# Kernel optimization log

Hardware: AMD Instinct MI355X
Metric: run time of the kernel (lower is better)

Reference implementation:

```python
import jax, jax.numpy as jnp
import numpy as np

B, N, D, H, K, L, BLOCKS = 8, 256, 768, 12, 128, 4, 2
HD = D // H
SCALING = HD ** -0.5
NEG = -1e9  # stand-in for -inf; exp underflows to exactly 0 in softmax


def layernorm(x, s, b):
    m = x.mean(-1, keepdims=True)
    v = ((x - m) ** 2).mean(-1, keepdims=True)
    return (x - m) * jax.lax.rsqrt(v + 1e-5) * s + b


def _gauss(x, mean, std):
    a = (2.0 * 3.14159) ** 0.5
    return jnp.exp(-0.5 * ((x - mean) / std) ** 2) / (a * std)


def setup_inputs() -> dict:
    key = jax.random.key(0)
    ks = jax.random.split(key, 16)
    nrm = lambda k, shape: jax.random.normal(k, shape, jnp.float32) * 0.02
    atoms = jax.random.randint(ks[0], (B, N), 0, 10, dtype=jnp.int32)
    pos = jax.random.normal(ks[1], (B, N, 3), jnp.float32)
    atom_emb = nrm(ks[2], (10, D)).at[0].set(0.0)  # padding_idx=0
    gbf_means = jax.random.uniform(ks[3], (K,), jnp.float32, 0.0, 3.0)
    gbf_stds = jax.random.uniform(ks[4], (K,), jnp.float32, 0.0, 3.0)
    gbf_mul = jnp.ones((100, 1), jnp.float32)
    gbf_bias = jnp.zeros((100, 1), jnp.float32)
    bp_w1 = nrm(ks[5], (K, K)); bp_b1 = jnp.zeros((K,), jnp.float32)
    bp_w2 = nrm(ks[6], (K, H)); bp_b2 = jnp.zeros((H,), jnp.float32)
    edge_w = nrm(ks[7], (K, D)); edge_b = jnp.zeros((D,), jnp.float32)
    ap_w = nrm(ks[8], (D, D)); ap_b = jnp.zeros((D,), jnp.float32)
    ln1_s = jnp.ones((L, D), jnp.float32); ln1_b = jnp.zeros((L, D), jnp.float32)
    wi = nrm(ks[9], (L, D, 3 * D)); bi = jnp.zeros((L, 3 * D), jnp.float32)
    wo = nrm(ks[10], (L, D, D)); bo = jnp.zeros((L, D), jnp.float32)
    ln2_s = jnp.ones((L, D), jnp.float32); ln2_b = jnp.zeros((L, D), jnp.float32)
    w1 = nrm(ks[11], (L, D, D)); b1 = jnp.zeros((L, D), jnp.float32)
    w2 = nrm(ks[12], (L, D, D)); b2 = jnp.zeros((L, D), jnp.float32)
    fln_s = jnp.ones((D,), jnp.float32); fln_b = jnp.zeros((D,), jnp.float32)
    return dict(atoms=atoms, pos=pos, atom_emb=atom_emb, gbf_means=gbf_means,
                gbf_stds=gbf_stds, gbf_mul=gbf_mul, gbf_bias=gbf_bias,
                bp_w1=bp_w1, bp_b1=bp_b1, bp_w2=bp_w2, bp_b2=bp_b2,
                edge_w=edge_w, edge_b=edge_b, ap_w=ap_w, ap_b=ap_b,
                ln1_s=ln1_s, ln1_b=ln1_b, wi=wi, bi=bi, wo=wo, bo=bo,
                ln2_s=ln2_s, ln2_b=ln2_b, w1=w1, b1=b1, w2=w2, b2=b2,
                fln_s=fln_s, fln_b=fln_b)


def reference(atoms, pos, atom_emb, gbf_means, gbf_stds, gbf_mul, gbf_bias,
              bp_w1, bp_b1, bp_w2, bp_b2, edge_w, edge_b, ap_w, ap_b,
              ln1_s, ln1_b, wi, bi, wo, bo, ln2_s, ln2_b, w1, b1, w2, b2,
              fln_s, fln_b):
    pad = atoms == 0  # [B,N]
    delta = pos[:, None, :, :] - pos[:, :, None, :]  # [B,N,N,3]
    sq = (delta * delta).sum(-1)
    dist = jnp.where(sq > 0, jnp.sqrt(jnp.where(sq > 0, sq, 1.0)), 0.0)  # safe sqrt
    et = atoms[:, :, None] * 10 + atoms[:, None, :]  # [B,N,N] in [0,100)
    e = gbf_mul[et] * dist[..., None] + gbf_bias[et]  # [B,N,N,1]
    gbf = _gauss(e, gbf_means, jnp.abs(gbf_stds) + 1e-5)  # [B,N,N,K]
    # zero out padded j-columns, sum over j -> per-node edge feature
    ef = jnp.where(pad[:, None, :, None], 0.0, gbf).sum(axis=2)  # [B,N,K]
    node = atom_emb[atoms] + ef @ edge_w + edge_b  # [B,N,D]
    x = jnp.swapaxes(node, 0, 1) @ ap_w + ap_b  # [N,B,D]
    # attention bias: K-dim Gaussian features -> per-head bias
    bias = jax.nn.gelu(gbf @ bp_w1 + bp_b1, approximate=False) @ bp_w2 + bp_b2  # [B,N,N,H]
    bias = jnp.transpose(bias, (0, 3, 1, 2))  # [B,H,N,N]
    bias = jnp.where(pad[:, None, None, :], NEG, bias)

    def body(x, p):
        s1, c1, Wi, Bi, Wo, Bo, s2, c2, W1, B1, W2, B2 = p
        h = layernorm(x, s1, c1)
        q, k, v = jnp.split(h @ Wi + Bi, 3, axis=-1)
        q = q.reshape(N, B, H, HD) * SCALING
        k = k.reshape(N, B, H, HD)
        v = v.reshape(N, B, H, HD)
        sc = jnp.einsum('ibhd,jbhd->bhij', q, k) + bias
        pA = jax.nn.softmax(sc, axis=-1)
        o = jnp.einsum('bhij,jbhd->ibhd', pA, v).reshape(N, B, D)
        x = x + o @ Wo + Bo
        h = layernorm(x, s2, c2)
        h = jax.nn.gelu(h @ W1 + B1, approximate=False) @ W2 + B2
        return x + h, None

    stacked = (ln1_s, ln1_b, wi, bi, wo, bo, ln2_s, ln2_b, w1, b1, w2, b2)
    for _ in range(BLOCKS):
        x, _ = jax.lax.scan(body, x, stacked)
    x = layernorm(x, fln_s, fln_b)
    return jnp.swapaxes(x, 0, 1)  # [B,N,D]
```

## Files before the change

kernel.cpp:

```cpp
#include <hip/hip_runtime.h>
#include <math.h>

constexpr int Bn = 8, Nn = 256, Dn = 768, Hn = 12, Kn = 128;
constexpr int Tn = Nn * Bn;
constexpr float SCALE = 0.125f;
constexpr float NEGB = -1e9f;
constexpr float INV768 = 1.0f / 768.0f;

typedef __attribute__((ext_vector_type(8))) short bf16x8;
typedef __attribute__((ext_vector_type(4))) float f32x4;

#define MFMA16(a, b, c) __builtin_amdgcn_mfma_f32_16x16x32_bf16((a), (b), (c), 0, 0, 0)

__device__ __forceinline__ void gload_lds16(const void* g, void* l) {
  __builtin_amdgcn_global_load_lds(
      (const __attribute__((address_space(1))) void*)g,
      (__attribute__((address_space(3))) void*)l, 16, 0, 0);
}

__device__ __forceinline__ ushort f2bf(float x) {
  union { float f; unsigned u; } v; v.f = x;
  unsigned r = (v.u + 0x7fff + ((v.u >> 16) & 1)) >> 16;
  return (ushort)r;
}
__device__ __forceinline__ ushort f2bf_t(float x) {
  union { float f; unsigned u; } v; v.f = x;
  return (ushort)(v.u >> 16);
}
__device__ __forceinline__ float bf2f(ushort u) {
  union { unsigned u; float f; } v; v.u = ((unsigned)u) << 16;
  return v.f;
}
__device__ __forceinline__ float gelu_fast(float x) {
  float u = x * (0.7978845608f + 0.0356774081f * x * x);
  float e = __expf(2.0f * u);
  float t = 1.0f - 2.0f / (e + 1.0f);
  return 0.5f * x * (1.0f + t);
}
__device__ __forceinline__ float wave_sum(float v) {
#pragma unroll
  for (int off = 32; off; off >>= 1) v += __shfl_xor(v, off);
  return v;
}

__global__ __launch_bounds__(256) void wtrans(const float* __restrict__ W,
                                              ushort* __restrict__ WT,
                                              int Kd, int Nd) {
  __shared__ float tile[64][65];
  const float* Wl = W + (size_t)blockIdx.z * Kd * Nd;
  ushort* WTl = WT + (size_t)blockIdx.z * Kd * Nd;
  int n0 = blockIdx.x * 64, k0 = blockIdx.y * 64;
  int tid = threadIdx.x;
  for (int e = tid; e < 64 * 64; e += 256) {
    int r = e >> 6, c = e & 63;
    tile[r][c] = Wl[(size_t)(k0 + r) * Nd + n0 + c];
  }
  __syncthreads();
  for (int e = tid; e < 64 * 64; e += 256) {
    int r = e >> 6, c = e & 63;
    WTl[(size_t)(n0 + r) * Kd + k0 + c] = f2bf(tile[c][r]);
  }
}

__global__ __launch_bounds__(128) void ef_kernel(
    const int* __restrict__ atoms, const float* __restrict__ pos,
    const float* __restrict__ means, const float* __restrict__ stds,
    const float* __restrict__ gmul, const float* __restrict__ gbias,
    ushort* __restrict__ ef) {
  int i = blockIdx.x, b = blockIdx.y;
  __shared__ float sj[Nn];
  __shared__ int padm[Nn];
  int tid = threadIdx.x;
  int ai = atoms[b * Nn + i];
  float px = pos[(b * Nn + i) * 3], py = pos[(b * Nn + i) * 3 + 1], pz = pos[(b * Nn + i) * 3 + 2];
  for (int j = tid; j < Nn; j += 128) {
    int aj = atoms[b * Nn + j];
    float dx = px - pos[(b * Nn + j) * 3];
    float dy = py - pos[(b * Nn + j) * 3 + 1];
    float dz = pz - pos[(b * Nn + j) * 3 + 2];
    float sq = dx * dx + dy * dy + dz * dz;
    float d = sq > 0.f ? sqrtf(sq) : 0.f;
    int et = ai * 10 + aj;
    sj[j] = fmaf(gmul[et], d, gbias[et]);
    padm[j] = (aj == 0);
  }
  __syncthreads();
  int k = tid;
  float mean = means[k];
  float sd = fabsf(stds[k]) + 1e-5f;
  float inv = 1.0f / sd;
  float cn = inv * 0.3989423f;
  float acc = 0.f;
  for (int j = 0; j < Nn; ++j) {
    if (padm[j]) continue;
    float t = (sj[j] - mean) * inv;
    acc += __expf(-0.5f * t * t);
  }
  ef[(size_t)(b * Nn + i) * Kn + k] = f2bf(acc * cn);
}

__global__ __launch_bounds__(256) void gbias_kernel(
    const int* __restrict__ atoms, const float* __restrict__ pos,
    const float* __restrict__ means, const float* __restrict__ stds,
    const float* __restrict__ gmul, const float* __restrict__ gbias_,
    const ushort* __restrict__ w1T, const float* __restrict__ b1,
    const float* __restrict__ w2, const float* __restrict__ b2,
    ushort* __restrict__ biasb) {
  int i = blockIdx.x, b = blockIdx.y;
  __shared__ char W1s[32768];
  __shared__ char Ag[16384];
  __shared__ char W2s[4096];
  __shared__ float sj[256];
  __shared__ int pml[256];
  __shared__ float b1s[128], invs_[128], mui[128], cns[128];
  const int tid = threadIdx.x, w = tid >> 6, ln = tid & 63;
  const int frow = ln & 15, fgrp = ln >> 4;
  {
    int srow = ln >> 4, sc = ln & 15;
#pragma unroll
    for (int q = 0; q < 8; ++q) {
      int inst = w * 8 + q;
      int row = inst * 4 + srow;
      const char* g = (const char*)(w1T + row * 128) + ((sc * 16) ^ ((row & 7) << 4));
      gload_lds16(g, W1s + inst * 1024);
    }
  }
  if (tid < 128) {
    float mean = means[tid];
    float sd = fabsf(stds[tid]) + 1e-5f;
    float inv = 1.0f / sd;
    invs_[tid] = inv;
    mui[tid] = mean * inv;
    cns[tid] = inv * 0.3989423f;
    b1s[tid] = b1[tid];
  }
  for (int e = tid; e < 2048; e += 256) {
    int h = e >> 7, k = e & 127;
    float v = (h < 12) ? w2[k * 12 + h] : 0.f;
    *(ushort*)(W2s + h * 256 + ((2 * k) ^ ((h & 7) << 4))) = f2bf(v);
  }
  {
    int ai = atoms[b * Nn + i];
    int j = tid;
    int aj = atoms[b * Nn + j];
    float dx = pos[(b * Nn + i) * 3]     - pos[(b * Nn + j) * 3];
    float dy = pos[(b * Nn + i) * 3 + 1] - pos[(b * Nn + j) * 3 + 1];
    float dz = pos[(b * Nn + i) * 3 + 2] - pos[(b * Nn + j) * 3 + 2];
    float sq = dx * dx + dy * dy + dz * dz;
    float d = sq > 0.f ? sqrtf(sq) : 0.f;
    int et = ai * 10 + aj;
    sj[j] = fmaf(gmul[et], d, gbias_[et]);
    pml[j] = (aj == 0);
  }
  __syncthreads();

  for (int jt = 0; jt < 4; ++jt) {
    int j0 = jt * 64;
    {
      int k = tid & 127;
      float inv = invs_[k], mu = mui[k], cn = cns[k];
      int r0 = (tid >> 7) * 32;
#pragma unroll 8
      for (int rr = 0; rr < 32; ++rr) {
        int row = r0 + rr;
        float t = fmaf(inv, sj[j0 + row], -mu);
        float g = __expf(-0.5f * t * t) * cn;
        *(ushort*)(Ag + row * 256 + ((2 * k) ^ ((row & 7) << 4))) = f2bf_t(g);
      }
    }
    __syncthreads();
    f32x4 acc[8] = {};
    const int arow = w * 16 + frow;
#pragma unroll
    for (int ks = 0; ks < 4; ++ks) {
      bf16x8 af = *(const bf16x8*)(Ag + arow * 256 + ((ks * 64 + fgrp * 16) ^ ((arow & 7) << 4)));
#pragma unroll
      for (int nt = 0; nt < 8; ++nt) {
        int brow = nt * 16 + frow;
        bf16x8 bfv = *(const bf16x8*)(W1s + brow * 256 + ((ks * 64 + fgrp * 16) ^ ((brow & 7) << 4)));
        acc[nt] = MFMA16(af, bfv, acc[nt]);
      }
    }
    __syncthreads();
#pragma unroll
    for (int nt = 0; nt < 8; ++nt) {
      int n = nt * 16 + frow;
#pragma unroll
      for (int r = 0; r < 4; ++r) {
        int jloc = w * 16 + fgrp * 4 + r;
        float g = gelu_fast(acc[nt][r] + b1s[n]);
        *(ushort*)(Ag + jloc * 256 + ((2 * n) ^ ((jloc & 7) << 4))) = f2bf_t(g);
      }
    }
    __syncthreads();
    {
      f32x4 acc2 = {};
      int jrow = w * 16 + frow;
#pragma unroll
      for (int ks = 0; ks < 4; ++ks) {
        bf16x8 af = *(const bf16x8*)(Ag + jrow * 256 + ((ks * 64 + fgrp * 16) ^ ((jrow & 7) << 4)));
        bf16x8 bfv = *(const bf16x8*)(W2s + frow * 256 + ((ks * 64 + fgrp * 16) ^ ((frow & 7) << 4)));
        acc2 = MFMA16(af, bfv, acc2);
      }
      if (frow < 12) {
        float bv = b2[frow];
#pragma unroll
        for (int r = 0; r < 4; ++r) {
          int jl = w * 16 + fgrp * 4 + r;
          int jg = j0 + jl;
          float v = pml[jg] ? NEGB : (acc2[r] + bv);
          biasb[(((size_t)b * Hn + frow) * Nn + i) * Nn + jg] = f2bf(v);
        }
      }
    }
    __syncthreads();
  }
}

template <int MODE>
__global__ __launch_bounds__(256, 4) void mgemm(
    const ushort* __restrict__ A, const ushort* __restrict__ WT,
    const float* __restrict__ bias, const float* __restrict__ res,
    void* __restrict__ Cout, const int* __restrict__ atomsp,
    const float* __restrict__ embp, int M, int Kd, int Nd) {
  __shared__ char smem[16384];
  char* ldsA = smem;
  char* ldsB = smem + 8192;
  const int tid = threadIdx.x, w = tid >> 6, ln = tid & 63;
  const int m0 = blockIdx.y * 64, n0 = blockIdx.x * 64;
  const int wm = (w >> 1) * 32, wn = (w & 1) * 32;
  const int srow = ln >> 3, schunk = ln & 7;
  const int sswz = (schunk * 16) ^ (srow << 4);
  const int frow = ln & 15, fgrp = ln >> 4;
  f32x4 acc[2][2] = {};
  for (int kt = 0; kt < Kd; kt += 64) {
    __syncthreads();
#pragma unroll
    for (int q = 0; q < 2; ++q) {
      int r = (w * 2 + q) * 8 + srow;
      gload_lds16((const char*)(A + (size_t)(m0 + r) * Kd + kt) + sswz, ldsA + (w * 2 + q) * 1024);
    }
#pragma unroll
    for (int q = 0; q < 2; ++q) {
      int r = (w * 2 + q) * 8 + srow;
      gload_lds16((const char*)(WT + (size_t)(n0 + r) * Kd + kt) + sswz, ldsB + (w * 2 + q) * 1024);
    }
    __syncthreads();
#pragma unroll
    for (int ks = 0; ks < 2; ++ks) {
      bf16x8 af[2], bfv[2];
#pragma unroll
      for (int mt = 0; mt < 2; ++mt) {
        int row = wm + mt * 16 + frow;
        af[mt] = *(const bf16x8*)(ldsA + row * 128 + ((ks * 64 + fgrp * 16) ^ ((row & 7) << 4)));
      }
#pragma unroll
      for (int nt = 0; nt < 2; ++nt) {
        int row = wn + nt * 16 + frow;
        bfv[nt] = *(const bf16x8*)(ldsB + row * 128 + ((ks * 64 + fgrp * 16) ^ ((row & 7) << 4)));
      }
      acc[0][0] = MFMA16(af[0], bfv[0], acc[0][0]);
      acc[0][1] = MFMA16(af[0], bfv[1], acc[0][1]);
      acc[1][0] = MFMA16(af[1], bfv[0], acc[1][0]);
      acc[1][1] = MFMA16(af[1], bfv[1], acc[1][1]);
    }
  }
#pragma unroll
  for (int nt = 0; nt < 2; ++nt) {
    int n = n0 + wn + nt * 16 + frow;
    float bv = bias[n];
#pragma unroll
    for (int mt = 0; mt < 2; ++mt) {
#pragma unroll
      for (int r = 0; r < 4; ++r) {
        int m = m0 + wm + mt * 16 + fgrp * 4 + r;
        float v = acc[mt][nt][r] + bv;
        if (MODE == 1) v = gelu_fast(v);
        if (MODE == 2) v += res[(size_t)m * Nd + n];
        if (MODE == 5) v += embp[(size_t)atomsp[m] * Nd + n];
        if (MODE == 2 || MODE == 3) ((float*)Cout)[(size_t)m * Nd + n] = v;
        else                        ((ushort*)Cout)[(size_t)m * Nd + n] = f2bf(v);
      }
    }
  }
}

__global__ __launch_bounds__(256, 2) void mgemm128_qkv(
    const ushort* __restrict__ A, const ushort* __restrict__ WT,
    const float* __restrict__ bias, ushort* __restrict__ vTout,
    ushort* __restrict__ Cout, int M, int Kd, int Nd) {
  __shared__ char smem[32768];
  char* ldsA = smem;
  char* ldsB = smem + 16384;
  const int tid = threadIdx.x, w = tid >> 6, ln = tid & 63;
  const int m0 = blockIdx.y * 128, n0 = blockIdx.x * 128;
  const int wm = (w >> 1) * 64, wn = (w & 1) * 64;
  const int srow = ln >> 3, schunk = ln & 7;
  const int sswz = (schunk * 16) ^ (srow << 4);
  const int frow = ln & 15, fgrp = ln >> 4;
  f32x4 acc[4][4] = {};
  for (int kt = 0; kt < Kd; kt += 64) {
    __syncthreads();
#pragma unroll
    for (int q = 0; q < 4; ++q) {
      int r = (w * 4 + q) * 8 + srow;
      gload_lds16((const char*)(A + (size_t)(m0 + r) * Kd + kt) + sswz, ldsA + (w * 4 + q) * 1024);
    }
#pragma unroll
    for (int q = 0; q < 4; ++q) {
      int r = (w * 4 + q) * 8 + srow;
      gload_lds16((const char*)(WT + (size_t)(n0 + r) * Kd + kt) + sswz, ldsB + (w * 4 + q) * 1024);
    }
    __syncthreads();
#pragma unroll
    for (int ks = 0; ks < 2; ++ks) {
      bf16x8 af[4], bfv[4];
#pragma unroll
      for (int mt = 0; mt < 4; ++mt) {
        int row = wm + mt * 16 + frow;
        af[mt] = *(const bf16x8*)(ldsA + row * 128 + ((ks * 64 + fgrp * 16) ^ ((row & 7) << 4)));
      }
#pragma unroll
      for (int nt = 0; nt < 4; ++nt) {
        int row = wn + nt * 16 + frow;
        bfv[nt] = *(const bf16x8*)(ldsB + row * 128 + ((ks * 64 + fgrp * 16) ^ ((row & 7) << 4)));
      }
#pragma unroll
      for (int mt = 0; mt < 4; ++mt)
#pragma unroll
        for (int nt = 0; nt < 4; ++nt)
          acc[mt][nt] = MFMA16(af[mt], bfv[nt], acc[mt][nt]);
    }
  }
#pragma unroll
  for (int nt = 0; nt < 4; ++nt) {
    int n = n0 + wn + nt * 16 + frow;
    float bv = bias[n];
    if (n >= 1536) {
      int dd = n - 1536, h = dd >> 6, d = dd & 63;
#pragma unroll
      for (int mt = 0; mt < 4; ++mt) {
#pragma unroll
        for (int r = 0; r < 4; ++r) {
          int m = m0 + wm + mt * 16 + fgrp * 4 + r;
          int bb = m >> 8, j = m & 255;
          vTout[(((size_t)bb * Hn + h) * 64 + d) * 256 + j] = f2bf(acc[mt][nt][r] + bv);
        }
      }
    } else {
      float sc = (n < 768) ? SCALE : 1.0f;
#pragma unroll
      for (int mt = 0; mt < 4; ++mt) {
#pragma unroll
        for (int r = 0; r < 4; ++r) {
          int m = m0 + wm + mt * 16 + fgrp * 4 + r;
          Cout[(size_t)m * Nd + n] = f2bf((acc[mt][nt][r] + bv) * sc);
        }
      }
    }
  }
}

__global__ __launch_bounds__(256, 2) void attn_mfma(
    const ushort* __restrict__ qkv, const ushort* __restrict__ vT,
    const ushort* __restrict__ biasb, ushort* __restrict__ Oout) {
  int it = blockIdx.x, h = blockIdx.y, b = blockIdx.z;
  int i0 = it * 64;
  __shared__ char smem[65536];
  char* Ks = smem;
  char* Vs = smem + 32768;
  const int tid = threadIdx.x, w = tid >> 6, ln = tid & 63;
  const int frow = ln & 15, fgrp = ln >> 4;
  {
    const int srow = ln >> 3, schunk = ln & 7;
#pragma unroll
    for (int q = 0; q < 8; ++q) {
      int inst = w * 8 + q;
      int row = inst * 8 + srow;
      const char* g = (const char*)(qkv + (size_t)(b * Nn + row) * 2304 + 768 + h * 64) +
                      ((schunk * 16) ^ ((row & 7) << 4));
      gload_lds16(g, Ks + inst * 1024);
    }
#pragma unroll
    for (int q = 0; q < 8; ++q) {
      int inst = w * 8 + q;
      int row = inst * 2 + (ln >> 5);
      int cb = (ln & 31) * 16;
      const char* g = (const char*)(vT + (size_t)((b * Hn + h) * 64 + row) * 256) +
                      (cb ^ ((row & 7) << 4));
      gload_lds16(g, Vs + inst * 1024);
    }
  }
  bf16x8 qf[2];
  {
    int qrow = i0 + w * 16 + frow;
    const ushort* qg = qkv + (size_t)(b * Nn + qrow) * 2304 + h * 64 + fgrp * 8;
    qf[0] = *(const bf16x8*)qg;
    qf[1] = *(const bf16x8*)(qg + 32);
  }
  __syncthreads();
  f32x4 s[16];
#pragma unroll
  for (int jtl = 0; jtl < 16; ++jtl) {
    int row = jtl * 16 + frow;
    const char* kb = Ks + row * 128;
    bf16x8 k0 = *(const bf16x8*)(kb + ((fgrp * 16) ^ ((row & 7) << 4)));
    bf16x8 k1 = *(const bf16x8*)(kb + ((64 + fgrp * 16) ^ ((row & 7) << 4)));
    f32x4 t = {};
    t = MFMA16(qf[0], k0, t);
    t = MFMA16(qf[1], k1, t);
    s[jtl] = t;
  }
  float inv[4];
#pragma unroll
  for (int r = 0; r < 4; ++r) {
    int i = i0 + w * 16 + fgrp * 4 + r;
    const ushort* brow = biasb + (((size_t)b * Hn + h) * Nn + i) * Nn;
    float su = 0.f;
#pragma unroll
    for (int jtl = 0; jtl < 16; ++jtl) {
      float p = __expf(s[jtl][r] + bf2f(brow[jtl * 16 + frow]));
      s[jtl][r] = p;
      su += p;
    }
    su += __shfl_xor(su, 1); su += __shfl_xor(su, 2);
    su += __shfl_xor(su, 4); su += __shfl_xor(su, 8);
    inv[r] = 1.0f / su;
  }
  __syncthreads();
  char* Ps = Ks + w * 8192;
#pragma unroll
  for (int r = 0; r < 4; ++r) {
    int prow = fgrp * 4 + r;
#pragma unroll
    for (int jtl = 0; jtl < 16; ++jtl) {
      int cb = jtl * 32 + frow * 2;
      *(ushort*)(Ps + prow * 512 + (cb ^ ((prow & 7) << 4))) = f2bf_t(s[jtl][r]);
    }
  }
  __syncthreads();
  bf16x8 pf[8];
#pragma unroll
  for (int ks = 0; ks < 8; ++ks)
    pf[ks] = *(const bf16x8*)(Ps + frow * 512 + ((ks * 64 + fgrp * 16) ^ ((frow & 7) << 4)));
  f32x4 o[4] = {};
#pragma unroll
  for (int dt = 0; dt < 4; ++dt) {
#pragma unroll
    for (int ks = 0; ks < 8; ++ks) {
      int row = dt * 16 + frow;
      bf16x8 vf = *(const bf16x8*)(Vs + row * 512 + ((ks * 64 + fgrp * 16) ^ ((row & 7) << 4)));
      o[dt] = MFMA16(pf[ks], vf, o[dt]);
    }
  }
#pragma unroll
  for (int dt = 0; dt < 4; ++dt)
#pragma unroll
    for (int r = 0; r < 4; ++r) {
      int i = i0 + w * 16 + fgrp * 4 + r;
      Oout[(size_t)(b * Nn + i) * Dn + h * 64 + dt * 16 + frow] = f2bf(o[dt][r] * inv[r]);
    }
}

template <int MODE>
__global__ __launch_bounds__(256) void ln_kernel(
    const float* __restrict__ x, const float* __restrict__ sc,
    const float* __restrict__ bi, void* __restrict__ out) {
  int t = blockIdx.x;
  int tid = threadIdx.x;
  const float* xr = x + (size_t)t * Dn;
  float v0 = xr[tid], v1 = xr[tid + 256], v2 = xr[tid + 512];
  __shared__ float red[4], red2[4];
  float s = wave_sum(v0 + v1 + v2);
  if ((tid & 63) == 0) red[tid >> 6] = s;
  __syncthreads();
  float mean = (red[0] + red[1] + red[2] + red[3]) * INV768;
  float d0 = v0 - mean, d1 = v1 - mean, d2 = v2 - mean;
  float vs = wave_sum(d0 * d0 + d1 * d1 + d2 * d2);
  if ((tid & 63) == 0) red2[tid >> 6] = vs;
  __syncthreads();
  float var = (red2[0] + red2[1] + red2[2] + red2[3]) * INV768;
  float r = rsqrtf(var + 1e-5f);
  if (MODE == 0) {
    ushort* o = (ushort*)out + (size_t)t * Dn;
    o[tid]       = f2bf(d0 * r * sc[tid]       + bi[tid]);
    o[tid + 256] = f2bf(d1 * r * sc[tid + 256] + bi[tid + 256]);
    o[tid + 512] = f2bf(d2 * r * sc[tid + 512] + bi[tid + 512]);
  } else {
    float* o = (float*)out + (size_t)t * Dn;
    o[tid]       = d0 * r * sc[tid]       + bi[tid];
    o[tid + 256] = d1 * r * sc[tid + 256] + bi[tid + 256];
    o[tid + 512] = d2 * r * sc[tid + 512] + bi[tid + 512];
  }
}

extern "C" void kernel_launch(void* const* d_in, const int* in_sizes, int n_in,
                              void* d_out, int out_size, void* d_ws, size_t ws_size,
                              hipStream_t stream) {
  (void)in_sizes; (void)n_in; (void)out_size; (void)ws_size;
  const int*   atoms    = (const int*)  d_in[0];
  const float* pos      = (const float*)d_in[1];
  const float* atom_emb = (const float*)d_in[2];
  const float* gbf_means= (const float*)d_in[3];
  const float* gbf_stds = (const float*)d_in[4];
  const float* gbf_mul  = (const float*)d_in[5];
  const float* gbf_bias = (const float*)d_in[6];
  const float* bp_w1    = (const float*)d_in[7];
  const float* bp_b1    = (const float*)d_in[8];
  const float* bp_w2    = (const float*)d_in[9];
  const float* bp_b2    = (const float*)d_in[10];
  const float* edge_w   = (const float*)d_in[11];
  const float* edge_b   = (const float*)d_in[12];
  const float* ap_w     = (const float*)d_in[13];
  const float* ap_b     = (const float*)d_in[14];
  const float* ln1_s    = (const float*)d_in[15];
  const float* ln1_b    = (const float*)d_in[16];
  const float* wi       = (const float*)d_in[17];
  const float* bi       = (const float*)d_in[18];
  const float* wo       = (const float*)d_in[19];
  const float* bo       = (const float*)d_in[20];
  const float* ln2_s    = (const float*)d_in[21];
  const float* ln2_b    = (const float*)d_in[22];
  const float* w1       = (const float*)d_in[23];
  const float* b1       = (const float*)d_in[24];
  const float* w2       = (const float*)d_in[25];
  const float* b2       = (const float*)d_in[26];
  const float* fln_s    = (const float*)d_in[27];
  const float* fln_b    = (const float*)d_in[28];
  float* out = (float*)d_out;

  ushort* wsb   = (ushort*)d_ws;
  ushort* biasb = wsb;
  ushort* qkvb  = biasb + (size_t)Bn * Hn * Nn * Nn;
  ushort* hb    = qkvb + (size_t)Tn * 2304;
  ushort* vT    = hb + (size_t)Tn * Dn;
  ushort* wiT   = vT + (size_t)Bn * Hn * 64 * 256;
  ushort* woT   = wiT + (size_t)4 * 2304 * Dn;
  ushort* w1T   = woT + (size_t)4 * Dn * Dn;
  ushort* w2T   = w1T + (size_t)4 * Dn * Dn;
  ushort* w1bT  = w2T + (size_t)4 * Dn * Dn;
  float*  xbuf  = (float*)(w1bT + 16384);
  ushort* apT   = qkvb;
  ushort* ewT   = qkvb + 589824;
  ushort* ffnb  = qkvb;
  ushort* efb   = vT;

  wtrans<<<dim3(12, 12, 1), 256, 0, stream>>>(ap_w, apT, 768, 768);
  wtrans<<<dim3(36, 12, 4), 256, 0, stream>>>(wi, wiT, 768, 2304);
  wtrans<<<dim3(12, 12, 4), 256, 0, stream>>>(wo, woT, 768, 768);
  wtrans<<<dim3(12, 12, 4), 256, 0, stream>>>(w1, w1T, 768, 768);
  wtrans<<<dim3(12, 12, 4), 256, 0, stream>>>(w2, w2T, 768, 768);
  wtrans<<<dim3(2, 2, 1), 256, 0, stream>>>(bp_w1, w1bT, 128, 128);
  wtrans<<<dim3(12, 2, 1), 256, 0, stream>>>(edge_w, ewT, 128, 768);

  dim3 gridNB(Nn, Bn);
  ef_kernel<<<gridNB, 128, 0, stream>>>(atoms, pos, gbf_means, gbf_stds, gbf_mul, gbf_bias, efb);
  gbias_kernel<<<gridNB, 256, 0, stream>>>(atoms, pos, gbf_means, gbf_stds,
                                           gbf_mul, gbf_bias, w1bT, bp_b1, bp_w2, bp_b2, biasb);
  mgemm<5><<<dim3(12, 32), 256, 0, stream>>>(efb, ewT, edge_b, nullptr, hb,
                                             atoms, atom_emb, Tn, 128, Dn);
  mgemm<3><<<dim3(12, 32), 256, 0, stream>>>(hb, apT, ap_b, nullptr, xbuf,
                                             nullptr, nullptr, Tn, Dn, Dn);

  for (int it = 0; it < 8; ++it) {
    int l = it & 3;
    ln_kernel<0><<<Tn, 256, 0, stream>>>(xbuf, ln1_s + l * Dn, ln1_b + l * Dn, hb);
    mgemm128_qkv<<<dim3(18, 16), 256, 0, stream>>>(hb, wiT + (size_t)l * 2304 * Dn,
                                                   bi + l * 2304, vT, qkvb, Tn, Dn, 2304);
    attn_mfma<<<dim3(4, Hn, Bn), 256, 0, stream>>>(qkvb, vT, biasb, hb);
    mgemm<2><<<dim3(12, 32), 256, 0, stream>>>(hb, woT + (size_t)l * Dn * Dn,
                                               bo + l * Dn, xbuf, xbuf,
                                               nullptr, nullptr, Tn, Dn, Dn);
    ln_kernel<0><<<Tn, 256, 0, stream>>>(xbuf, ln2_s + l * Dn, ln2_b + l * Dn, hb);
    mgemm<1><<<dim3(12, 32), 256, 0, stream>>>(hb, w1T + (size_t)l * Dn * Dn,
                                               b1 + l * Dn, nullptr, ffnb,
                                               nullptr, nullptr, Tn, Dn, Dn);
    mgemm<2><<<dim3(12, 32), 256, 0, stream>>>(ffnb, w2T + (size_t)l * Dn * Dn,
                                               b2 + l * Dn, xbuf, xbuf,
                                               nullptr, nullptr, Tn, Dn, Dn);
  }
  ln_kernel<1><<<Tn, 256, 0, stream>>>(xbuf, fln_s, fln_b, out);
}
```

Before: 754.3 us.

## Fuse edge-feature Gaussian sum into attention-bias kernel and precompute quadratic exponent

Removes the separate ef_kernel and computes the padded-masked Gaussian edge-feature sums inside gbias_kernel, reusing the Gaussian values it already evaluates for the bias MLP. The exponent is rewritten as a precomputed quadratic A*s^2+B*s+C per k, and each thread now handles two adjacent k values with packed bf16 stores. The goal is to drop one kernel launch and the duplicated N*N*K exp work. The cost is a final cross-thread reduction through LDS and some change in rounding, since the exponent is now expanded rather than squared after centering.

```diff
diff --git a/kernel.cpp b/kernel.cpp
--- a/kernel.cpp
+++ b/kernel.cpp
@@ -30,6 +30,9 @@
 __device__ __forceinline__ float bf2f(ushort u) {
   union { unsigned u; float f; } v; v.u = ((unsigned)u) << 16;
   return v.f;
+}
+__device__ __forceinline__ unsigned pk2(float a, float b) {
+  return (unsigned)f2bf_t(a) | ((unsigned)f2bf_t(b) << 16);
 }
 __device__ __forceinline__ float gelu_fast(float x) {
   float u = x * (0.7978845608f + 0.0356774081f * x * x);
@@ -62,57 +65,20 @@
   }
 }
 
-__global__ __launch_bounds__(128) void ef_kernel(
-    const int* __restrict__ atoms, const float* __restrict__ pos,
-    const float* __restrict__ means, const float* __restrict__ stds,
-    const float* __restrict__ gmul, const float* __restrict__ gbias,
-    ushort* __restrict__ ef) {
-  int i = blockIdx.x, b = blockIdx.y;
-  __shared__ float sj[Nn];
-  __shared__ int padm[Nn];
-  int tid = threadIdx.x;
-  int ai = atoms[b * Nn + i];
-  float px = pos[(b * Nn + i) * 3], py = pos[(b * Nn + i) * 3 + 1], pz = pos[(b * Nn + i) * 3 + 2];
-  for (int j = tid; j < Nn; j += 128) {
-    int aj = atoms[b * Nn + j];
-    float dx = px - pos[(b * Nn + j) * 3];
-    float dy = py - pos[(b * Nn + j) * 3 + 1];
-    float dz = pz - pos[(b * Nn + j) * 3 + 2];
-    float sq = dx * dx + dy * dy + dz * dz;
-    float d = sq > 0.f ? sqrtf(sq) : 0.f;
-    int et = ai * 10 + aj;
-    sj[j] = fmaf(gmul[et], d, gbias[et]);
-    padm[j] = (aj == 0);
-  }
-  __syncthreads();
-  int k = tid;
-  float mean = means[k];
-  float sd = fabsf(stds[k]) + 1e-5f;
-  float inv = 1.0f / sd;
-  float cn = inv * 0.3989423f;
-  float acc = 0.f;
-  for (int j = 0; j < Nn; ++j) {
-    if (padm[j]) continue;
-    float t = (sj[j] - mean) * inv;
-    acc += __expf(-0.5f * t * t);
-  }
-  ef[(size_t)(b * Nn + i) * Kn + k] = f2bf(acc * cn);
-}
-
 __global__ __launch_bounds__(256) void gbias_kernel(
     const int* __restrict__ atoms, const float* __restrict__ pos,
     const float* __restrict__ means, const float* __restrict__ stds,
     const float* __restrict__ gmul, const float* __restrict__ gbias_,
     const ushort* __restrict__ w1T, const float* __restrict__ b1,
     const float* __restrict__ w2, const float* __restrict__ b2,
-    ushort* __restrict__ biasb) {
+    ushort* __restrict__ biasb, ushort* __restrict__ efb) {
   int i = blockIdx.x, b = blockIdx.y;
   __shared__ char W1s[32768];
   __shared__ char Ag[16384];
   __shared__ char W2s[4096];
   __shared__ float sj[256];
   __shared__ int pml[256];
-  __shared__ float b1s[128], invs_[128], mui[128], cns[128];
+  __shared__ float b1s[128], kA[128], kB[128], kC[128], kcns[128];
   const int tid = threadIdx.x, w = tid >> 6, ln = tid & 63;
   const int frow = ln & 15, fgrp = ln >> 4;
   {
@@ -129,9 +95,11 @@
     float mean = means[tid];
     float sd = fabsf(stds[tid]) + 1e-5f;
     float inv = 1.0f / sd;
-    invs_[tid] = inv;
-    mui[tid] = mean * inv;
-    cns[tid] = inv * 0.3989423f;
+    float A = -0.5f * inv * inv;
+    kA[tid] = A;
+    kB[tid] = -2.0f * A * mean;
+    kC[tid] = A * mean * mean;
+    kcns[tid] = inv * 0.3989423f;
     b1s[tid] = b1[tid];
   }
   for (int e = tid; e < 2048; e += 256) {
@@ -154,19 +122,25 @@
   }
   __syncthreads();
 
+  const int kp = tid & 63, rquad = tid >> 6;
+  const int k0i = 2 * kp, k1i = 2 * kp + 1;
+  const float A0 = kA[k0i], B0 = kB[k0i], C0 = kC[k0i], cn0 = kcns[k0i];
+  const float A1 = kA[k1i], B1 = kB[k1i], C1 = kC[k1i], cn1 = kcns[k1i];
+  float facc0 = 0.f, facc1 = 0.f;
+
   for (int jt = 0; jt < 4; ++jt) {
     int j0 = jt * 64;
-    {
-      int k = tid & 127;
-      float inv = invs_[k], mu = mui[k], cn = cns[k];
-      int r0 = (tid >> 7) * 32;
-#pragma unroll 8
-      for (int rr = 0; rr < 32; ++rr) {
-        int row = r0 + rr;
-        float t = fmaf(inv, sj[j0 + row], -mu);
-        float g = __expf(-0.5f * t * t) * cn;
-        *(ushort*)(Ag + row * 256 + ((2 * k) ^ ((row & 7) << 4))) = f2bf_t(g);
-      }
+#pragma unroll
+    for (int rr = 0; rr < 16; ++rr) {
+      int row = rquad * 16 + rr;
+      int jg = j0 + row;
+      float s = sj[jg];
+      float e0 = __expf(fmaf(fmaf(A0, s, B0), s, C0));
+      float e1 = __expf(fmaf(fmaf(A1, s, B1), s, C1));
+      int padj = pml[jg];
+      facc0 += padj ? 0.f : e0;
+      facc1 += padj ? 0.f : e1;
+      *(unsigned*)(Ag + row * 256 + ((4 * kp) ^ ((row & 7) << 4))) = pk2(e0 * cn0, e1 * cn1);
     }
     __syncthreads();
     f32x4 acc[8] = {};
@@ -214,6 +188,18 @@
       }
     }
     __syncthreads();
+  }
+  {
+    float* efp = (float*)Ag;
+    efp[(kp * 4 + rquad) * 2 + 0] = facc0;
+    efp[(kp * 4 + rquad) * 2 + 1] = facc1;
+    __syncthreads();
+    if (tid < 128) {
+      int k = tid, kq = k >> 1, lo = k & 1;
+      float s = efp[(kq * 4 + 0) * 2 + lo] + efp[(kq * 4 + 1) * 2 + lo] +
+                efp[(kq * 4 + 2) * 2 + lo] + efp[(kq * 4 + 3) * 2 + lo];
+      efb[(size_t)(b * Nn + i) * Kn + k] = f2bf(s * kcns[k]);
+    }
   }
 }
 
@@ -554,9 +540,9 @@
   wtrans<<<dim3(12, 2, 1), 256, 0, stream>>>(edge_w, ewT, 128, 768);
 
   dim3 gridNB(Nn, Bn);
-  ef_kernel<<<gridNB, 128, 0, stream>>>(atoms, pos, gbf_means, gbf_stds, gbf_mul, gbf_bias, efb);
   gbias_kernel<<<gridNB, 256, 0, stream>>>(atoms, pos, gbf_means, gbf_stds,
-                                           gbf_mul, gbf_bias, w1bT, bp_b1, bp_w2, bp_b2, biasb);
+                                           gbf_mul, gbf_bias, w1bT, bp_b1, bp_w2, bp_b2,
+                                           biasb, efb);
   mgemm<5><<<dim3(12, 32), 256, 0, stream>>>(efb, ewT, edge_b, nullptr, hb,
                                              atoms, atom_emb, Tn, 128, Dn);
   mgemm<3><<<dim3(12, 32), 256, 0, stream>>>(hb, apT, ap_b, nullptr, xbuf,
```

New measurement: 728.9 us. 3.4% less time.
